# Kernel optimization log

Measured on AMD Instinct MI355X. Metric: run time of the kernel, lower is better.

## Reference

```python
import jax, jax.numpy as jnp
import numpy as np
import math

MAX_DELAY = 25
TAU = 2.0
VTH = 1.0
BN_EPS = 1e-5
ATAN_ALPHA = 2.0


def build_dcls_kernel(W, P, SIG, D):
    # Gaussian-interpolated DCLS kernel ('gauss' version).
    # W, P, SIG: (O, I, K) -> kernel (O, I, D)
    lim = D // 2
    j = jnp.arange(D, dtype=W.dtype)                      # (D,)
    Pc = jnp.clip(P, -lim, lim) + lim                     # (O, I, K)
    sig = jnp.abs(SIG) + 0.27
    g = jnp.exp(-0.5 * ((j - Pc[..., None]) / sig[..., None]) ** 2)  # (O,I,K,D)
    g = g / (g.sum(-1, keepdims=True) + 1e-7)
    return jnp.einsum('oik,oikd->oid', W, g)


def dcls_conv_positive(x, W, P, SIG, D):
    # Dale-positive: abs(weight) before kernel construction; padding=0 (VALID)
    k = build_dcls_kernel(jnp.abs(W), P, SIG, D)
    return jax.lax.conv_general_dilated(
        x, k, window_strides=(1,), padding='VALID',
        dimension_numbers=('NCW', 'OIW', 'NCW'))


def batchnorm_m(x, gamma, beta):
    # spikingjelly layer.BatchNorm1d step_mode='m' on (T, B, C):
    # flattens (T*B) as batch, normalizes per channel (training-mode stats).
    mean = x.mean(axis=(0, 1))
    var = x.var(axis=(0, 1))
    return (x - mean) * jax.lax.rsqrt(var + BN_EPS) * gamma + beta


def lif_multistep(x_seq, tau, v_th):
    # LIFNode, decay_input=False, v_reset=0 (hard reset), detach_reset=True,
    # ATan surrogate. x_seq: (T, B, C).
    inv_tau = jnp.asarray(1.0 / tau, x_seq.dtype)
    def step(v, xt):
        v = v * (1.0 - inv_tau) + xt              # charge (decay_input=False)
        u = v - v_th
        sg = jnp.arctan(0.5 * math.pi * ATAN_ALPHA * u) / math.pi + 0.5
        hard = (u >= 0).astype(xt.dtype)
        spike = sg + jax.lax.stop_gradient(hard - sg)
        v = v * (1.0 - jax.lax.stop_gradient(spike))   # hard reset, detached
        return v, spike
    v0 = jnp.zeros(x_seq.shape[1:], x_seq.dtype)
    _, spikes = jax.lax.scan(step, v0, x_seq)
    return spikes


def setup_inputs() -> dict:
    key = jax.random.key(0)
    ks = jax.random.split(key, 8)
    B, C_in, T = 64, 700, 300
    n_out, n_inh, K = 256, 128, 1
    return {
        'x': jax.random.normal(ks[0], (B, C_in, T), jnp.float32),
        'W_inh': jax.random.normal(ks[1], (n_inh, C_in, K), jnp.float32),
        'P_inh': jax.random.normal(ks[2], (n_inh, C_in, K), jnp.float32),
        'SIG_inh': jax.random.uniform(ks[3], (n_inh, C_in, K), jnp.float32),
        'W_exc': jax.random.normal(ks[4], (n_out, C_in, K), jnp.float32),
        'P_exc': jax.random.normal(ks[5], (n_out, C_in, K), jnp.float32),
        'SIG_exc': jax.random.uniform(ks[6], (n_out, C_in, K), jnp.float32),
        'w_exc_inh': jax.random.uniform(ks[7], (n_out, n_inh), jnp.float32),
        'bn_gamma': jnp.ones((n_inh,), jnp.float32),
        'bn_beta': jnp.zeros((n_inh,), jnp.float32),
    }


def reference(x, W_inh, P_inh, SIG_inh, W_exc, P_exc, SIG_exc, w_exc_inh,
              bn_gamma, bn_beta):
    # inhibitory branch
    in_inhib = dcls_conv_positive(x, W_inh, P_inh, SIG_inh, MAX_DELAY)  # (B,Ci,T')
    in_inhib = jnp.transpose(in_inhib, (2, 0, 1))                       # (T',B,Ci)
    in_inhib = batchnorm_m(in_inhib, bn_gamma, bn_beta)
    spikes = lif_multistep(in_inhib, TAU, VTH)                          # (T',B,Ci)
    out_inhib = jnp.einsum('tbi,oi->tbo', spikes, -jnp.abs(w_exc_inh))
    out_inhib = jnp.transpose(out_inhib, (1, 2, 0))                     # (B,O,T')
    # excitatory branch
    excit = dcls_conv_positive(x, W_exc, P_exc, SIG_exc, MAX_DELAY)     # (B,O,T')
    return excit + out_inhib
```

## Files before the change

### kernel.cpp

```cpp
#include <hip/hip_runtime.h>
#include <math.h>

#define CI   700
#define TIN  300
#define DD   25
#define TOUT 276
#define BB   64
#define OINH 128
#define OEXC 256

#define TROWS 312
#define IPAD  704

typedef __attribute__((ext_vector_type(8))) short short8;
typedef __attribute__((ext_vector_type(4))) float f32x4;
typedef __attribute__((ext_vector_type(8))) unsigned short ushort8v;

static __device__ __forceinline__ unsigned short f2bf(float f) {
    unsigned int u = __float_as_uint(f);
    unsigned int r = (u + 0x7FFFu + ((u >> 16) & 1u)) >> 16;
    return (unsigned short)r;
}
static __device__ __forceinline__ float bf2f(unsigned short h) {
    return __uint_as_float(((unsigned int)h) << 16);
}

static __device__ __forceinline__ void gload_lds16(const void* g, void* l) {
    __builtin_amdgcn_global_load_lds(
        (const __attribute__((address_space(1))) unsigned int*)g,
        (__attribute__((address_space(3))) unsigned int*)l, 16, 0, 0);
}

__global__ void build_kt(const float* __restrict__ W, const float* __restrict__ P,
                         const float* __restrict__ SIG, float* __restrict__ kt, int O) {
    int n = blockIdx.x * 256 + threadIdx.x;
    if (n >= O * CI) return;
    int o = n % O;
    int i = n / O;
    float w   = fabsf(W[o * CI + i]);
    float p   = fminf(fmaxf(P[o * CI + i], -12.f), 12.f) + 12.f;
    float sig = fabsf(SIG[o * CI + i]) + 0.27f;
    float inv = 1.f / sig;
    float g[DD];
    float sum = 0.f;
#pragma unroll
    for (int d = 0; d < DD; ++d) {
        float e = ((float)d - p) * inv;
        g[d] = expf(-0.5f * e * e);
        sum += g[d];
    }
    float sc = w / (sum + 1e-7f);
#pragma unroll
    for (int d = 0; d < DD; ++d)
        kt[(i * DD + d) * O + o] = g[d] * sc;
}

__global__ void kexc_build(const float* __restrict__ W, const float* __restrict__ P,
                           const float* __restrict__ SIG, unsigned short* __restrict__ kb2) {
    int n = blockIdx.x * 256 + threadIdx.x;
    if (n >= OEXC * IPAD) return;
    int o = n / IPAD, ip = n % IPAD;
    if (ip >= CI) {
#pragma unroll
        for (int d = 0; d < DD; ++d)
            kb2[((size_t)d * OEXC + o) * IPAD + ip] = 0;
        return;
    }
    float w   = fabsf(W[o * CI + ip]);
    float p   = fminf(fmaxf(P[o * CI + ip], -12.f), 12.f) + 12.f;
    float sig = fabsf(SIG[o * CI + ip]) + 0.27f;
    float inv = 1.f / sig;
    float g[DD];
    float sum = 0.f;
#pragma unroll
    for (int d = 0; d < DD; ++d) {
        float e = ((float)d - p) * inv;
        g[d] = expf(-0.5f * e * e);
        sum += g[d];
    }
    float sc = w / (sum + 1e-7f);
#pragma unroll
    for (int d = 0; d < DD; ++d)
        kb2[((size_t)d * OEXC + o) * IPAD + ip] = f2bf(g[d] * sc);
}

__global__ void kinh_build(const float* __restrict__ W, const float* __restrict__ P,
                           const float* __restrict__ SIG,
                           unsigned short* __restrict__ kbh, unsigned short* __restrict__ kbl) {
    int n = blockIdx.x * 256 + threadIdx.x;
    if (n >= OINH * IPAD) return;
    int o = n / IPAD, ip = n % IPAD;
    if (ip >= CI) {
#pragma unroll
        for (int d = 0; d < DD; ++d) {
            kbh[((size_t)d * OINH + o) * IPAD + ip] = 0;
            kbl[((size_t)d * OINH + o) * IPAD + ip] = 0;
        }
        return;
    }
    float w   = fabsf(W[o * CI + ip]);
    float p   = fminf(fmaxf(P[o * CI + ip], -12.f), 12.f) + 12.f;
    float sig = fabsf(SIG[o * CI + ip]) + 0.27f;
    float inv = 1.f / sig;
    float g[DD];
    float sum = 0.f;
#pragma unroll
    for (int d = 0; d < DD; ++d) {
        float e = ((float)d - p) * inv;
        g[d] = expf(-0.5f * e * e);
        sum += g[d];
    }
    float sc = w / (sum + 1e-7f);
#pragma unroll
    for (int d = 0; d < DD; ++d) {
        float v = g[d] * sc;
        unsigned short h = f2bf(v);
        kbh[((size_t)d * OINH + o) * IPAD + ip] = h;
        kbl[((size_t)d * OINH + o) * IPAD + ip] = f2bf(v - bf2f(h));
    }
}

__global__ __launch_bounds__(256)
void xt_kernel(const float* __restrict__ x, unsigned short* __restrict__ xTh,
               unsigned short* __restrict__ xTl) {
    __shared__ float tile[64][65];
    const int tid = threadIdx.x;
    const int t0 = blockIdx.x * 64, i0 = blockIdx.y * 64, b = blockIdx.z;
#pragma unroll
    for (int s = 0; s < 16; ++s) {
        int f = s * 256 + tid;
        int tt = f & 63, ii = f >> 6;
        float v = 0.f;
        if (t0 + tt < TIN && i0 + ii < CI)
            v = x[((size_t)b * CI + i0 + ii) * TIN + t0 + tt];
        tile[tt][ii] = v;
    }
    __syncthreads();
#pragma unroll
    for (int s = 0; s < 2; ++s) {
        int f = s * 256 + tid;
        int tt = f >> 3, g = f & 7;
        if (t0 + tt < TROWS) {
            ushort8v vh, vl;
#pragma unroll
            for (int e = 0; e < 8; ++e) {
                float v = tile[tt][g * 8 + e];
                unsigned short h = f2bf(v);
                vh[e] = h;
                vl[e] = f2bf(v - bf2f(h));
            }
            size_t off = ((size_t)b * TROWS + t0 + tt) * IPAD + i0 + g * 8;
            *(ushort8v*)(xTh + off) = vh;
            if (xTl) *(ushort8v*)(xTl + off) = vl;
        }
    }
}

__global__ void wt_kernel(const float* __restrict__ w, float* __restrict__ wt) {
    int n = blockIdx.x * 256 + threadIdx.x;
    if (n >= OINH * OEXC) return;
    int o = n % OEXC, c = n / OEXC;
    wt[c * OEXC + o] = -fabsf(w[o * OINH + c]);
}

__global__ __launch_bounds__(128)
void conv_fused32(const unsigned short* __restrict__ xTh, const unsigned short* __restrict__ xTl,
                  const unsigned short* __restrict__ kb2,
                  const unsigned short* __restrict__ kbh, const unsigned short* __restrict__ kbl,
                  float* __restrict__ pexc0, float* __restrict__ pexc1,
                  float* __restrict__ pinh0, float* __restrict__ pinh1) {
    __shared__ unsigned short lds[16384];

    const int tid  = threadIdx.x;
    const int wave = tid >> 6;
    const int lane = tid & 63;
    const int l15 = lane & 15, l4 = lane >> 4;
    const int tt   = blockIdx.x % 3;
    const int ksp  = blockIdx.x / 3;
    const int role = blockIdx.y;
    const int b    = blockIdx.z;
    const int t0   = tt * 96;
    const int icb  = ksp * 11;

    const int ld_r = lane >> 2;
    const int ld_c = (((lane & 3) ^ ((lane >> 3) & 3)) << 4);
    const int SA   = (l15 >> 1) & 3;

    const size_t xstride = (size_t)IPAD * 2;
    const char* xh_base = (const char*)xTh + ((size_t)b * TROWS + t0) * xstride;
    const char* xl_base = (const char*)xTl + ((size_t)b * TROWS + t0) * xstride;

    if (role < 2) {
        unsigned short* xs = lds;
        unsigned short* ks = lds + 4096;
        const int o0 = role * 128 + wave * 64;

        f32x4 acc[4][6];
#pragma unroll
        for (int i = 0; i < 4; ++i)
#pragma unroll
            for (int j = 0; j < 6; ++j) acc[i][j] = (f32x4)0.f;

        for (int c = 0; c < 11; ++c) {
            const size_t cb = (size_t)(icb + c) * 64;
            __syncthreads();
            for (int j = wave; j < 8; j += 2)
                gload_lds16(xh_base + (size_t)(16 * j + ld_r) * xstride + cb + ld_c,
                            (char*)xs + j * 1024);
            {
                const char* kbase = (const char*)kb2 + (size_t)o0 * xstride + cb;
                char* kdst = (char*)(ks + wave * 2048);
#pragma unroll
                for (int j = 0; j < 4; ++j)
                    gload_lds16(kbase + (size_t)(16 * j + ld_r) * xstride + ld_c,
                                kdst + j * 1024);
            }
            asm volatile("s_waitcnt vmcnt(0)" ::: "memory");
            __syncthreads();

            for (int d = 0; d < DD; ++d) {
                const int cur = d & 1;
                if (d < DD - 1) {
                    const char* kbase = (const char*)kb2 +
                        ((size_t)((d + 1) * OEXC) + o0) * xstride + cb;
                    char* kdst = (char*)(ks + ((cur ^ 1) * 2 + wave) * 2048);
#pragma unroll
                    for (int j = 0; j < 4; ++j)
                        gload_lds16(kbase + (size_t)(16 * j + ld_r) * xstride + ld_c,
                                    kdst + j * 1024);
                }
                const char* kp = (const char*)(ks + (cur * 2 + wave) * 2048);
                short8 A[4];
#pragma unroll
                for (int i = 0; i < 4; ++i)
                    A[i] = *(const short8*)(kp + (i * 16 + l15) * 64 + ((l4 ^ SA) << 4));
#pragma unroll
                for (int j = 0; j < 6; ++j) {
                    const int tr = j * 16 + l15 + d;
                    short8 Bv = *(const short8*)((const char*)xs + tr * 64 +
                                                 ((l4 ^ ((tr >> 1) & 3)) << 4));
#pragma unroll
                    for (int i = 0; i < 4; ++i)
                        acc[i][j] = __builtin_amdgcn_mfma_f32_16x16x32_bf16(
                            A[i], Bv, acc[i][j], 0, 0, 0);
                }
                asm volatile("s_waitcnt vmcnt(0)" ::: "memory");
            }
        }
        float* dst = ksp ? pexc1 : pexc0;
#pragma unroll
        for (int i = 0; i < 4; ++i)
#pragma unroll
            for (int j = 0; j < 6; ++j) {
                const int t = t0 + j * 16 + l15;
                if (t < TOUT) {
                    float* op = dst + ((size_t)b * OEXC + o0 + i * 16 + l4 * 4) * TOUT + t;
#pragma unroll
                    for (int r = 0; r < 4; ++r) op[(size_t)r * TOUT] = acc[i][j][r];
                }
            }
    } else {
        unsigned short* xsh = lds;
        unsigned short* xsl = lds + 4096;
        unsigned short* ksh = lds + 8192;
        unsigned short* ksl = lds + 12288;
        const int o0  = (role - 2) * 64;
        const int wtb = wave * 48;

        f32x4 acc[4][3];
#pragma unroll
        for (int i = 0; i < 4; ++i)
#pragma unroll
            for (int j = 0; j < 3; ++j) acc[i][j] = (f32x4)0.f;

        const unsigned short* kb = wave ? kbl : kbh;

        for (int c = 0; c < 11; ++c) {
            const size_t cb = (size_t)(icb + c) * 64;
            __syncthreads();
            for (int j = wave; j < 8; j += 2) {
                gload_lds16(xh_base + (size_t)(16 * j + ld_r) * xstride + cb + ld_c,
                            (char*)xsh + j * 1024);
                gload_lds16(xl_base + (size_t)(16 * j + ld_r) * xstride + cb + ld_c,
                            (char*)xsl + j * 1024);
            }
            {
                const char* kbase = (const char*)kb + (size_t)o0 * xstride + cb;
                char* kdst = (char*)((wave ? ksl : ksh));
#pragma unroll
                for (int j = 0; j < 4; ++j)
                    gload_lds16(kbase + (size_t)(16 * j + ld_r) * xstride + ld_c,
                                kdst + j * 1024);
            }
            asm volatile("s_waitcnt vmcnt(0)" ::: "memory");
            __syncthreads();

            for (int d = 0; d < DD; ++d) {
                const int cur = d & 1;
                if (d < DD - 1) {
                    const char* kbase = (const char*)kb +
                        ((size_t)((d + 1) * OINH) + o0) * xstride + cb;
                    char* kdst = (char*)((wave ? ksl : ksh) + (cur ^ 1) * 2048);
#pragma unroll
                    for (int j = 0; j < 4; ++j)
                        gload_lds16(kbase + (size_t)(16 * j + ld_r) * xstride + ld_c,
                                    kdst + j * 1024);
                }
                const char* kph = (const char*)(ksh + cur * 2048);
                const char* kpl = (const char*)(ksl + cur * 2048);
                short8 Ah[4], Al[4];
#pragma unroll
                for (int i = 0; i < 4; ++i) {
                    Ah[i] = *(const short8*)(kph + (i * 16 + l15) * 64 + ((l4 ^ SA) << 4));
                    Al[i] = *(const short8*)(kpl + (i * 16 + l15) * 64 + ((l4 ^ SA) << 4));
                }
#pragma unroll
                for (int j = 0; j < 3; ++j) {
                    const int tr = wtb + j * 16 + l15 + d;
                    const int xo = tr * 64 + ((l4 ^ ((tr >> 1) & 3)) << 4);
                    short8 Bh = *(const short8*)((const char*)xsh + xo);
                    short8 Bl = *(const short8*)((const char*)xsl + xo);
#pragma unroll
                    for (int i = 0; i < 4; ++i) {
                        acc[i][j] = __builtin_amdgcn_mfma_f32_16x16x32_bf16(
                            Ah[i], Bh, acc[i][j], 0, 0, 0);
                        acc[i][j] = __builtin_amdgcn_mfma_f32_16x16x32_bf16(
                            Ah[i], Bl, acc[i][j], 0, 0, 0);
                        acc[i][j] = __builtin_amdgcn_mfma_f32_16x16x32_bf16(
                            Al[i], Bh, acc[i][j], 0, 0, 0);
                    }
                }
                asm volatile("s_waitcnt vmcnt(0)" ::: "memory");
                __syncthreads();
            }
        }
        float* dst = ksp ? pinh1 : pinh0;
#pragma unroll
        for (int i = 0; i < 4; ++i)
#pragma unroll
            for (int j = 0; j < 3; ++j) {
                const int t = t0 + wtb + j * 16 + l15;
                if (t < TOUT) {
                    float* op = dst + ((size_t)b * OINH + o0 + i * 16 + l4 * 4) * TOUT + t;
#pragma unroll
                    for (int r = 0; r < 4; ++r) op[(size_t)r * TOUT] = acc[i][j][r];
                }
            }
    }
}

__global__ void add_exc(const float* __restrict__ p1, float* __restrict__ out) {
    int n = blockIdx.x * 256 + threadIdx.x;
    float4 a = ((const float4*)out)[n];
    float4 v = ((const float4*)p1)[n];
    a.x += v.x; a.y += v.y; a.z += v.z; a.w += v.w;
    ((float4*)out)[n] = a;
}

__global__ void bn_stats2(float* __restrict__ cinh, const float* __restrict__ q1,
                          const float* __restrict__ gamma, const float* __restrict__ beta,
                          float* __restrict__ scale, float* __restrict__ shift) {
    const int c = blockIdx.x, tid = threadIdx.x;
    float sum = 0.f, sq = 0.f;
    for (int idx = tid; idx < BB * TOUT; idx += 256) {
        int b = idx / TOUT, t = idx - b * TOUT;
        size_t off = (size_t)(b * OINH + c) * TOUT + t;
        float v = cinh[off] + q1[off];
        cinh[off] = v;
        sum += v; sq += v * v;
    }
#pragma unroll
    for (int off = 32; off; off >>= 1) {
        sum += __shfl_down(sum, off);
        sq  += __shfl_down(sq, off);
    }
    __shared__ float ls[8];
    int wid = tid >> 6;
    if ((tid & 63) == 0) { ls[wid * 2] = sum; ls[wid * 2 + 1] = sq; }
    __syncthreads();
    if (tid == 0) {
        float S = 0.f, Q = 0.f;
#pragma unroll
        for (int wv = 0; wv < 4; ++wv) { S += ls[wv * 2]; Q += ls[wv * 2 + 1]; }
        const float n = (float)(BB * TOUT);
        float mean = S / n;
        float var  = Q / n - mean * mean;
        float rs   = 1.f / sqrtf(var + 1e-5f);
        float sc   = gamma[c] * rs;
        scale[c] = sc;
        shift[c] = beta[c] - mean * sc;
    }
}

__global__ __launch_bounds__(128)
void conv_mfma(const unsigned short* __restrict__ xTh, const unsigned short* __restrict__ kb2,
               float* __restrict__ out) {
    __shared__ unsigned short xs[120 * 64];
    __shared__ unsigned short ks[2][2][64 * 64];

    const int tid  = threadIdx.x;
    const int wave = tid >> 6;
    const int lane = tid & 63;
    const int l15 = lane & 15, l4 = lane >> 4, l7 = lane & 7;
    const int b  = blockIdx.z;
    const int t0 = blockIdx.x * 96;
    const int o0 = blockIdx.y * 128 + wave * 64;

    const int ld_row = lane >> 3;
    const int ld_swz = ((l7 ^ ld_row) << 4);

    f32x4 acc[4][6];
#pragma unroll
    for (int i = 0; i < 4; ++i)
#pragma unroll
        for (int j = 0; j < 6; ++j) acc[i][j] = (f32x4)0.f;

    const char* xrow0 = (const char*)xTh + ((size_t)b * TROWS + t0) * (IPAD * 2);

    for (int ic = 0; ic < 11; ++ic) {
        const int ic0 = ic * 64;
        __syncthreads();
        for (int j = wave; j < 15; j += 2)
            gload_lds16(xrow0 + (size_t)(8 * j + ld_row) * (IPAD * 2) + ic0 * 2 + ld_swz,
                        (char*)xs + j * 1024);
        {
            const char* ksrc = (const char*)kb2 + ((size_t)o0) * (IPAD * 2) + ic0 * 2;
            char* kdst = (char*)ks + (0 * 2 + wave) * 8192;
#pragma unroll
            for (int j = 0; j < 8; ++j)
                gload_lds16(ksrc + (size_t)(8 * j + ld_row) * (IPAD * 2) + ld_swz,
                            kdst + j * 1024);
        }
        asm volatile("s_waitcnt vmcnt(0)" ::: "memory");
        __syncthreads();

        for (int d = 0; d < DD; ++d) {
            const int cur = d & 1;
            if (d < DD - 1) {
                const char* ksrc = (const char*)kb2 +
                    ((size_t)(d + 1) * OEXC + o0) * (IPAD * 2) + ic0 * 2;
                char* kdst = (char*)ks + ((cur ^ 1) * 2 + wave) * 8192;
#pragma unroll
                for (int j = 0; j < 8; ++j)
                    gload_lds16(ksrc + (size_t)(8 * j + ld_row) * (IPAD * 2) + ld_swz,
                                kdst + j * 1024);
            }
            const char* kp = (const char*)ks + (cur * 2 + wave) * 8192;
#pragma unroll
            for (int ks2 = 0; ks2 < 2; ++ks2) {
                const int cg = ks2 * 4 + l4;
                short8 A[4];
#pragma unroll
                for (int i = 0; i < 4; ++i)
                    A[i] = *(const short8*)(kp + (i * 16 + l15) * 128 + ((cg ^ l7) << 4));
#pragma unroll
                for (int j = 0; j < 6; ++j) {
                    const int tr = j * 16 + l15 + d;
                    short8 Bv = *(const short8*)((const char*)xs + tr * 128 +
                                                 ((cg ^ (tr & 7)) << 4));
#pragma unroll
                    for (int i = 0; i < 4; ++i)
                        acc[i][j] = __builtin_amdgcn_mfma_f32_16x16x32_bf16(
                            A[i], Bv, acc[i][j], 0, 0, 0);
                }
            }
            asm volatile("s_waitcnt vmcnt(0)" ::: "memory");
        }
    }

#pragma unroll
    for (int i = 0; i < 4; ++i)
#pragma unroll
        for (int j = 0; j < 6; ++j) {
            const int tt = t0 + j * 16 + l15;
            if (tt < TOUT) {
                float* op = out + ((size_t)b * OEXC + o0 + i * 16 + l4 * 4) * TOUT + tt;
#pragma unroll
                for (int r = 0; r < 4; ++r) op[(size_t)r * TOUT] = acc[i][j][r];
            }
        }
}

__global__ __launch_bounds__(128)
void conv_mfma_inh(const unsigned short* __restrict__ xTh, const unsigned short* __restrict__ xTl,
                   const unsigned short* __restrict__ kbh, const unsigned short* __restrict__ kbl,
                   float* __restrict__ cinh) {
    __shared__ unsigned short xsh[120 * 64];
    __shared__ unsigned short xsl[120 * 64];
    __shared__ unsigned short ksh[2][64 * 64];
    __shared__ unsigned short ksl[2][64 * 64];

    const int tid  = threadIdx.x;
    const int wave = tid >> 6;
    const int lane = tid & 63;
    const int l15 = lane & 15, l4 = lane >> 4, l7 = lane & 7;
    const int b  = blockIdx.z;
    const int t0 = blockIdx.x * 96;
    const int o0 = blockIdx.y * 64;
    const int wtb = wave * 48;

    const int ld_row = lane >> 3;
    const int ld_swz = ((l7 ^ ld_row) << 4);

    f32x4 acc[4][3];
#pragma unroll
    for (int i = 0; i < 4; ++i)
#pragma unroll
        for (int j = 0; j < 3; ++j) acc[i][j] = (f32x4)0.f;

    const char* xrh = (const char*)xTh + ((size_t)b * TROWS + t0) * (IPAD * 2);
    const char* xrl = (const char*)xTl + ((size_t)b * TROWS + t0) * (IPAD * 2);
    const unsigned short* kb = wave ? kbl : kbh;

    for (int ic = 0; ic < 11; ++ic) {
        const int ic0 = ic * 64;
        __syncthreads();
        for (int j = wave; j < 15; j += 2) {
            gload_lds16(xrh + (size_t)(8 * j + ld_row) * (IPAD * 2) + ic0 * 2 + ld_swz,
                        (char*)xsh + j * 1024);
            gload_lds16(xrl + (size_t)(8 * j + ld_row) * (IPAD * 2) + ic0 * 2 + ld_swz,
                        (char*)xsl + j * 1024);
        }
        {
            char* kd = wave ? (char*)ksl[0] : (char*)ksh[0];
#pragma unroll
            for (int j = 0; j < 8; ++j)
                gload_lds16((const char*)kb +
                                ((size_t)(0 * OINH + o0 + 8 * j + ld_row)) * (IPAD * 2) +
                                ic0 * 2 + ld_swz,
                            kd + j * 1024);
        }
        asm volatile("s_waitcnt vmcnt(0)" ::: "memory");
        __syncthreads();

        for (int d = 0; d < DD; ++d) {
            const int cur = d & 1;
            if (d < DD - 1) {
                char* kd = wave ? (char*)ksl[cur ^ 1] : (char*)ksh[cur ^ 1];
#pragma unroll
                for (int j = 0; j < 8; ++j)
                    gload_lds16((const char*)kb +
                                    ((size_t)((d + 1) * OINH + o0 + 8 * j + ld_row)) * (IPAD * 2) +
                                    ic0 * 2 + ld_swz,
                                kd + j * 1024);
            }
            const char* kph = (const char*)ksh[cur];
            const char* kpl = (const char*)ksl[cur];
#pragma unroll
            for (int k2 = 0; k2 < 2; ++k2) {
                const int cg = k2 * 4 + l4;
                short8 Ah[4], Al[4];
#pragma unroll
                for (int i = 0; i < 4; ++i) {
                    Ah[i] = *(const short8*)(kph + (i * 16 + l15) * 128 + ((cg ^ l7) << 4));
                    Al[i] = *(const short8*)(kpl + (i * 16 + l15) * 128 + ((cg ^ l7) << 4));
                }
#pragma unroll
                for (int j = 0; j < 3; ++j) {
                    const int tr = wtb + j * 16 + l15 + d;
                    short8 Bh = *(const short8*)((const char*)xsh + tr * 128 +
                                                 ((cg ^ (tr & 7)) << 4));
                    short8 Bl = *(const short8*)((const char*)xsl + tr * 128 +
                                                 ((cg ^ (tr & 7)) << 4));
#pragma unroll
                    for (int i = 0; i < 4; ++i) {
                        acc[i][j] = __builtin_amdgcn_mfma_f32_16x16x32_bf16(
                            Ah[i], Bh, acc[i][j], 0, 0, 0);
                        acc[i][j] = __builtin_amdgcn_mfma_f32_16x16x32_bf16(
                            Ah[i], Bl, acc[i][j], 0, 0, 0);
                        acc[i][j] = __builtin_amdgcn_mfma_f32_16x16x32_bf16(
                            Al[i], Bh, acc[i][j], 0, 0, 0);
                    }
                }
            }
            asm volatile("s_waitcnt vmcnt(0)" ::: "memory");
            __syncthreads();
        }
    }

#pragma unroll
    for (int i = 0; i < 4; ++i)
#pragma unroll
        for (int j = 0; j < 3; ++j) {
            const int tt = t0 + wtb + j * 16 + l15;
            if (tt < TOUT) {
                float* op = cinh + ((size_t)b * OINH + o0 + i * 16 + l4 * 4) * TOUT + tt;
#pragma unroll
                for (int r = 0; r < 4; ++r) op[(size_t)r * TOUT] = acc[i][j][r];
            }
        }
}

__global__ __launch_bounds__(256)
void conv_dcls(const float* __restrict__ x, const float* __restrict__ kt,
               float* __restrict__ out, int O) {
    __shared__ float k_lds[100 * 128];
    __shared__ float x_lds[4 * 88];

    const int tid = threadIdx.x;
    const int tx = tid & 7;
    const int ty = tid >> 3;
    const int b  = blockIdx.z;
    const int t0 = blockIdx.x * 64;
    const int o0 = blockIdx.y * 128;
    const int tlim = TIN - t0;

    float acc[4][8];
#pragma unroll
    for (int ro = 0; ro < 4; ++ro)
#pragma unroll
        for (int rt = 0; rt < 8; ++rt) acc[ro][rt] = 0.f;

    for (int chunk = 0; chunk < 175; ++chunk) {
        const int i0 = chunk * 4;
        __syncthreads();
#pragma unroll
        for (int s = 0; s < 13; ++s) {
            int f = tid + s * 256;
            if (f < 3200) {
                int j = f >> 5, o4 = f & 31;
                ((float4*)k_lds)[f] =
                    *(const float4*)(kt + (size_t)(i0 * DD + j) * O + o0 + o4 * 4);
            }
        }
        if (tid < 88) {
            int icc = tid / 22, wq = tid % 22;
            float4 v = make_float4(0.f, 0.f, 0.f, 0.f);
            if (wq * 4 < tlim)
                v = *(const float4*)(x + (size_t)(b * CI + i0 + icc) * TIN + t0 + wq * 4);
            ((float4*)x_lds)[tid] = v;
        }
        __syncthreads();
#pragma unroll
        for (int icc = 0; icc < 4; ++icc) {
            float xv[32];
#pragma unroll
            for (int wq = 0; wq < 8; ++wq)
                *(float4*)(xv + 4 * wq) = ((const float4*)(x_lds + icc * 88))[tx * 2 + wq];
#pragma unroll
            for (int d = 0; d < DD; ++d) {
                float4 kv = ((const float4*)(k_lds + (icc * DD + d) * 128))[ty];
                float kvv[4] = {kv.x, kv.y, kv.z, kv.w};
#pragma unroll
                for (int ro = 0; ro < 4; ++ro)
#pragma unroll
                    for (int rt = 0; rt < 8; ++rt)
                        acc[ro][rt] += kvv[ro] * xv[rt + d];
            }
        }
    }
    const int tvalid = TOUT - t0;
#pragma unroll
    for (int ro = 0; ro < 4; ++ro) {
        float* op = out + (size_t)(b * O + o0 + ty * 4 + ro) * TOUT + t0;
#pragma unroll
        for (int u = 0; u < 2; ++u) {
            int toff = tx * 8 + u * 4;
            if (toff < tvalid) {
                float4 v = make_float4(acc[ro][u * 4 + 0], acc[ro][u * 4 + 1],
                                       acc[ro][u * 4 + 2], acc[ro][u * 4 + 3]);
                *(float4*)(op + toff) = v;
            }
        }
    }
}

__global__ void bn_stats(const float* __restrict__ cinh, const float* __restrict__ gamma,
                         const float* __restrict__ beta, float* __restrict__ scale,
                         float* __restrict__ shift) {
    const int c = blockIdx.x, tid = threadIdx.x;
    float sum = 0.f, sq = 0.f;
    for (int idx = tid; idx < BB * TOUT; idx += 256) {
        int b = idx / TOUT, t = idx - b * TOUT;
        float v = cinh[(size_t)(b * OINH + c) * TOUT + t];
        sum += v; sq += v * v;
    }
#pragma unroll
    for (int off = 32; off; off >>= 1) {
        sum += __shfl_down(sum, off);
        sq  += __shfl_down(sq, off);
    }
    __shared__ float ls[8];
    int wid = tid >> 6;
    if ((tid & 63) == 0) { ls[wid * 2] = sum; ls[wid * 2 + 1] = sq; }
    __syncthreads();
    if (tid == 0) {
        float S = 0.f, Q = 0.f;
#pragma unroll
        for (int wv = 0; wv < 4; ++wv) { S += ls[wv * 2]; Q += ls[wv * 2 + 1]; }
        const float n = (float)(BB * TOUT);
        float mean = S / n;
        float var  = Q / n - mean * mean;
        float rs   = 1.f / sqrtf(var + 1e-5f);
        float sc   = gamma[c] * rs;
        scale[c] = sc;
        shift[c] = beta[c] - mean * sc;
    }
}

__global__ void lif_kernel(const float* __restrict__ cinh, const float* __restrict__ scale,
                           const float* __restrict__ shift, unsigned char* __restrict__ spk) {
    const int b = blockIdx.x, c = threadIdx.x;
    const float sc = scale[c], sh = shift[c];
    const float* row = cinh + (size_t)(b * OINH + c) * TOUT;
    float v = 0.f;
    for (int t = 0; t < TOUT; ++t) {
        float xin = row[t] * sc + sh;
        v = 0.5f * v + xin;
        unsigned char s = (v >= 1.f) ? 1 : 0;
        spk[((size_t)t * BB + b) * OINH + c] = s;
        v = (v >= 1.f) ? 0.f : v;
    }
}

__global__ __launch_bounds__(256)
void finale(const unsigned char* __restrict__ spk, const float* __restrict__ wt,
            float* __restrict__ out) {
    __shared__ float s_lds[64 * 129];
    const int tid = threadIdx.x;
    const int tx = tid & 15, ty = tid >> 4;
    const int b = blockIdx.z, t0 = blockIdx.x * 64, o0 = blockIdx.y * 64;

#pragma unroll
    for (int s = 0; s < 32; ++s) {
        int f = tid + s * 256;
        int tt = f >> 7, c = f & 127;
        float v = 0.f;
        if (t0 + tt < TOUT) v = (float)spk[((size_t)(t0 + tt) * BB + b) * OINH + c];
        s_lds[tt * 129 + c] = v;
    }
    __syncthreads();

    float acc[4][4] = {{0.f}};
#pragma unroll 4
    for (int c = 0; c < 128; ++c) {
        float4 wv = *(const float4*)(wt + c * OEXC + o0 + ty * 4);
        float wvv[4] = {wv.x, wv.y, wv.z, wv.w};
        float sv[4];
#pragma unroll
        for (int rt = 0; rt < 4; ++rt) sv[rt] = s_lds[(tx * 4 + rt) * 129 + c];
#pragma unroll
        for (int ro = 0; ro < 4; ++ro)
#pragma unroll
            for (int rt = 0; rt < 4; ++rt)
                acc[ro][rt] += wvv[ro] * sv[rt];
    }

    const int tvalid = TOUT - t0;
    if (tx * 4 < tvalid) {
#pragma unroll
        for (int ro = 0; ro < 4; ++ro) {
            float* op = out + (size_t)(b * OEXC + o0 + ty * 4 + ro) * TOUT + t0 + tx * 4;
            float4 v = *(float4*)op;
            v.x += acc[ro][0]; v.y += acc[ro][1]; v.z += acc[ro][2]; v.w += acc[ro][3];
            *(float4*)op = v;
        }
    }
}

extern "C" void kernel_launch(void* const* d_in, const int* in_sizes, int n_in,
                              void* d_out, int out_size, void* d_ws, size_t ws_size,
                              hipStream_t stream) {
    const float* x       = (const float*)d_in[0];
    const float* W_inh   = (const float*)d_in[1];
    const float* P_inh   = (const float*)d_in[2];
    const float* SIG_inh = (const float*)d_in[3];
    const float* W_exc   = (const float*)d_in[4];
    const float* P_exc   = (const float*)d_in[5];
    const float* SIG_exc = (const float*)d_in[6];
    const float* w_ei    = (const float*)d_in[7];
    const float* gamma   = (const float*)d_in[8];
    const float* beta    = (const float*)d_in[9];
    float* out = (float*)d_out;

    const size_t XT_ELEMS   = (size_t)BB * TROWS * IPAD;
    const size_t KEXC_ELEMS = (size_t)DD * OEXC * IPAD;
    const size_t KINH_ELEMS = (size_t)DD * OINH * IPAD;
    const size_t CINH_ELEMS = (size_t)BB * OINH * TOUT;
    const size_t PEXC_ELEMS = (size_t)BB * OEXC * TOUT;

    const size_t NEED_FAST = 2 * XT_ELEMS * 2 + KEXC_ELEMS * 2 + 2 * KINH_ELEMS * 2 +
                             CINH_ELEMS * 4 + OINH * OEXC * 4 + CINH_ELEMS;
    const size_t NEED_FAST2 = (2 * XT_ELEMS + KEXC_ELEMS + 2 * KINH_ELEMS) * 2 +
                              (PEXC_ELEMS + 2 * CINH_ELEMS + OINH * OEXC + 256) * 4 +
                              CINH_ELEMS;

    if (ws_size >= NEED_FAST2) {
        unsigned short* xTh = (unsigned short*)d_ws;
        unsigned short* xTl = xTh + XT_ELEMS;
        unsigned short* kb2 = xTl + XT_ELEMS;
        unsigned short* kbh = kb2 + KEXC_ELEMS;
        unsigned short* kbl = kbh + KINH_ELEMS;
        float* pexc1 = (float*)(kbl + KINH_ELEMS);
        float* cinh  = pexc1 + PEXC_ELEMS;
        float* pinh1 = cinh + CINH_ELEMS;
        float* wt    = pinh1 + CINH_ELEMS;
        float* scale = wt + OINH * OEXC;
        float* shift = scale + OINH;
        unsigned char* spk = (unsigned char*)(shift + OINH);

        hipLaunchKernelGGL(kexc_build, dim3((OEXC * IPAD + 255) / 256), dim3(256), 0, stream,
                           W_exc, P_exc, SIG_exc, kb2);
        hipLaunchKernelGGL(kinh_build, dim3((OINH * IPAD + 255) / 256), dim3(256), 0, stream,
                           W_inh, P_inh, SIG_inh, kbh, kbl);
        hipLaunchKernelGGL(xt_kernel, dim3(5, 11, 64), dim3(256), 0, stream, x, xTh, xTl);
        hipLaunchKernelGGL(wt_kernel, dim3(128), dim3(256), 0, stream, w_ei, wt);

        hipLaunchKernelGGL(conv_fused32, dim3(6, 4, 64), dim3(128), 0, stream,
                           xTh, xTl, kb2, kbh, kbl, out, pexc1, cinh, pinh1);

        hipLaunchKernelGGL(add_exc, dim3((unsigned)(PEXC_ELEMS / 4 / 256)), dim3(256), 0, stream,
                           pexc1, out);
        hipLaunchKernelGGL(bn_stats2, dim3(128), dim3(256), 0, stream,
                           cinh, pinh1, gamma, beta, scale, shift);
        hipLaunchKernelGGL(lif_kernel, dim3(64), dim3(128), 0, stream, cinh, scale, shift, spk);
        hipLaunchKernelGGL(finale, dim3(5, 4, 64), dim3(256), 0, stream, spk, wt, out);
    } else if (ws_size >= NEED_FAST) {
        unsigned short* xTh = (unsigned short*)d_ws;
        unsigned short* xTl = xTh + XT_ELEMS;
        unsigned short* kb2 = xTl + XT_ELEMS;
        unsigned short* kbh = kb2 + KEXC_ELEMS;
        unsigned short* kbl = kbh + KINH_ELEMS;
        float* cinh  = (float*)(kbl + KINH_ELEMS);
        float* wt    = cinh + CINH_ELEMS;
        float* scale = wt + OINH * OEXC;
        float* shift = scale + OINH;
        unsigned char* spk = (unsigned char*)(shift + OINH);

        hipLaunchKernelGGL(kexc_build, dim3((OEXC * IPAD + 255) / 256), dim3(256), 0, stream,
                           W_exc, P_exc, SIG_exc, kb2);
        hipLaunchKernelGGL(kinh_build, dim3((OINH * IPAD + 255) / 256), dim3(256), 0, stream,
                           W_inh, P_inh, SIG_inh, kbh, kbl);
        hipLaunchKernelGGL(xt_kernel, dim3(5, 11, 64), dim3(256), 0, stream, x, xTh, xTl);
        hipLaunchKernelGGL(wt_kernel, dim3(128), dim3(256), 0, stream, w_ei, wt);

        hipLaunchKernelGGL(conv_mfma, dim3(3, 2, 64), dim3(128), 0, stream, xTh, kb2, out);
        hipLaunchKernelGGL(conv_mfma_inh, dim3(3, 2, 64), dim3(128), 0, stream,
                           xTh, xTl, kbh, kbl, cinh);

        hipLaunchKernelGGL(bn_stats, dim3(128), dim3(256), 0, stream, cinh, gamma, beta, scale, shift);
        hipLaunchKernelGGL(lif_kernel, dim3(64), dim3(128), 0, stream, cinh, scale, shift, spk);
        hipLaunchKernelGGL(finale, dim3(5, 4, 64), dim3(256), 0, stream, spk, wt, out);
    } else {
        unsigned short* xTh = (unsigned short*)d_ws;
        unsigned short* kb2 = xTh + XT_ELEMS;
        float* kt_inh = (float*)(kb2 + KEXC_ELEMS);
        float* cinh   = kt_inh + 2240000;
        float* wt     = cinh + CINH_ELEMS;
        float* scale  = wt + OINH * OEXC;
        float* shift  = scale + OINH;
        unsigned char* spk = (unsigned char*)(shift + OINH);

        hipLaunchKernelGGL(kexc_build, dim3((OEXC * IPAD + 255) / 256), dim3(256), 0, stream,
                           W_exc, P_exc, SIG_exc, kb2);
        hipLaunchKernelGGL(build_kt, dim3(350), dim3(256), 0, stream,
                           W_inh, P_inh, SIG_inh, kt_inh, OINH);
        hipLaunchKernelGGL(xt_kernel, dim3(5, 11, 64), dim3(256), 0, stream, x, xTh,
                           (unsigned short*)nullptr);
        hipLaunchKernelGGL(wt_kernel, dim3(128), dim3(256), 0, stream, w_ei, wt);

        hipLaunchKernelGGL(conv_mfma, dim3(3, 2, 64), dim3(128), 0, stream, xTh, kb2, out);
        hipLaunchKernelGGL(conv_dcls, dim3(5, 1, 64), dim3(256), 0, stream, x, kt_inh, cinh, OINH);

        hipLaunchKernelGGL(bn_stats, dim3(128), dim3(256), 0, stream, cinh, gamma, beta, scale, shift);
        hipLaunchKernelGGL(lif_kernel, dim3(64), dim3(128), 0, stream, cinh, scale, shift, spk);
        hipLaunchKernelGGL(finale, dim3(5, 4, 64), dim3(256), 0, stream, spk, wt, out);
    }
}
```

Before: 548.2 us.

## Triple-buffer kernel prefetch and rebalance inhibitory MFMA tiling; tile LIF input through LDS

The fused conv kernel now keeps three LDS kernel buffers and prefetches two delay steps ahead, waiting with a partial vmcnt so loads overlap the MFMA work. The inhibitory path splits output channels across the two waves, each computing the hi/lo split over the full 96-step tile, instead of splitting time, and drops a per-delay __syncthreads. A new LIF kernel stages input chunks through padded LDS so global reads are coalesced. Costs are more LDS per block, which may reduce occupancy, plus some reshuffling of fallback code.

```diff
diff --git a/kernel.cpp b/kernel.cpp
--- a/kernel.cpp
+++ b/kernel.cpp
@@ -164,12 +164,12 @@
 }
 
 __global__ __launch_bounds__(128)
-void conv_fused32(const unsigned short* __restrict__ xTh, const unsigned short* __restrict__ xTl,
-                  const unsigned short* __restrict__ kb2,
-                  const unsigned short* __restrict__ kbh, const unsigned short* __restrict__ kbl,
-                  float* __restrict__ pexc0, float* __restrict__ pexc1,
-                  float* __restrict__ pinh0, float* __restrict__ pinh1) {
-    __shared__ unsigned short lds[16384];
+void conv_fused_v3(const unsigned short* __restrict__ xTh, const unsigned short* __restrict__ xTl,
+                   const unsigned short* __restrict__ kb2,
+                   const unsigned short* __restrict__ kbh, const unsigned short* __restrict__ kbl,
+                   float* __restrict__ pexc0, float* __restrict__ pexc1,
+                   float* __restrict__ pinh0, float* __restrict__ pinh1) {
+    __shared__ unsigned short lds[20480];
 
     const int tid  = threadIdx.x;
     const int wave = tid >> 6;
@@ -207,29 +207,31 @@
             for (int j = wave; j < 8; j += 2)
                 gload_lds16(xh_base + (size_t)(16 * j + ld_r) * xstride + cb + ld_c,
                             (char*)xs + j * 1024);
-            {
-                const char* kbase = (const char*)kb2 + (size_t)o0 * xstride + cb;
-                char* kdst = (char*)(ks + wave * 2048);
+#pragma unroll
+            for (int q = 0; q < 2; ++q) {
+                const char* kbase = (const char*)kb2 + ((size_t)(q * OEXC) + o0) * xstride + cb;
+                char* kdst = (char*)ks + (q * 2 + wave) * 4096;
 #pragma unroll
                 for (int j = 0; j < 4; ++j)
                     gload_lds16(kbase + (size_t)(16 * j + ld_r) * xstride + ld_c,
                                 kdst + j * 1024);
             }
-            asm volatile("s_waitcnt vmcnt(0)" ::: "memory");
+            asm volatile("s_waitcnt vmcnt(4)" ::: "memory");
             __syncthreads();
 
+            int cur = 0;
             for (int d = 0; d < DD; ++d) {
-                const int cur = d & 1;
-                if (d < DD - 1) {
+                if (d < DD - 2) {
+                    int nb = cur + 2; if (nb >= 3) nb -= 3;
                     const char* kbase = (const char*)kb2 +
-                        ((size_t)((d + 1) * OEXC) + o0) * xstride + cb;
-                    char* kdst = (char*)(ks + ((cur ^ 1) * 2 + wave) * 2048);
+                        ((size_t)((d + 2) * OEXC) + o0) * xstride + cb;
+                    char* kdst = (char*)ks + (nb * 2 + wave) * 4096;
 #pragma unroll
                     for (int j = 0; j < 4; ++j)
                         gload_lds16(kbase + (size_t)(16 * j + ld_r) * xstride + ld_c,
                                     kdst + j * 1024);
                 }
-                const char* kp = (const char*)(ks + (cur * 2 + wave) * 2048);
+                const char* kp = (const char*)ks + (cur * 2 + wave) * 4096;
                 short8 A[4];
 #pragma unroll
                 for (int i = 0; i < 4; ++i)
@@ -244,7 +246,11 @@
                         acc[i][j] = __builtin_amdgcn_mfma_f32_16x16x32_bf16(
                             A[i], Bv, acc[i][j], 0, 0, 0);
                 }
-                asm volatile("s_waitcnt vmcnt(0)" ::: "memory");
+                if (d < DD - 2)
+                    asm volatile("s_waitcnt vmcnt(4)" ::: "memory");
+                else if (d == DD - 2)
+                    asm volatile("s_waitcnt vmcnt(0)" ::: "memory");
+                cur = (cur == 2) ? 0 : cur + 1;
             }
         }
         float* dst = ksp ? pexc1 : pexc0;
@@ -262,18 +268,15 @@
     } else {
         unsigned short* xsh = lds;
         unsigned short* xsl = lds + 4096;
-        unsigned short* ksh = lds + 8192;
-        unsigned short* ksl = lds + 12288;
+        unsigned short* kws = lds + 8192;
         const int o0  = (role - 2) * 64;
-        const int wtb = wave * 48;
-
-        f32x4 acc[4][3];
-#pragma unroll
-        for (int i = 0; i < 4; ++i)
-#pragma unroll
-            for (int j = 0; j < 3; ++j) acc[i][j] = (f32x4)0.f;
-
-        const unsigned short* kb = wave ? kbl : kbh;
+        const int o0w = o0 + wave * 32;
+
+        f32x4 acc[2][6];
+#pragma unroll
+        for (int i = 0; i < 2; ++i)
+#pragma unroll
+            for (int j = 0; j < 6; ++j) acc[i][j] = (f32x4)0.f;
 
         for (int c = 0; c < 11; ++c) {
             const size_t cb = (size_t)(icb + c) * 64;
@@ -284,44 +287,50 @@
                 gload_lds16(xl_base + (size_t)(16 * j + ld_r) * xstride + cb + ld_c,
                             (char*)xsl + j * 1024);
             }
-            {
-                const char* kbase = (const char*)kb + (size_t)o0 * xstride + cb;
-                char* kdst = (char*)((wave ? ksl : ksh));
-#pragma unroll
-                for (int j = 0; j < 4; ++j)
-                    gload_lds16(kbase + (size_t)(16 * j + ld_r) * xstride + ld_c,
+#pragma unroll
+            for (int q = 0; q < 2; ++q) {
+                const size_t ko = ((size_t)(q * OINH) + o0w) * xstride + cb;
+                char* kdst = (char*)kws + (q * 2 + wave) * 4096;
+#pragma unroll
+                for (int j = 0; j < 2; ++j) {
+                    gload_lds16((const char*)kbh + ko + (size_t)(16 * j + ld_r) * xstride + ld_c,
                                 kdst + j * 1024);
-            }
-            asm volatile("s_waitcnt vmcnt(0)" ::: "memory");
+                    gload_lds16((const char*)kbl + ko + (size_t)(16 * j + ld_r) * xstride + ld_c,
+                                kdst + 2048 + j * 1024);
+                }
+            }
+            asm volatile("s_waitcnt vmcnt(4)" ::: "memory");
             __syncthreads();
 
+            int cur = 0;
             for (int d = 0; d < DD; ++d) {
-                const int cur = d & 1;
-                if (d < DD - 1) {
-                    const char* kbase = (const char*)kb +
-                        ((size_t)((d + 1) * OINH) + o0) * xstride + cb;
-                    char* kdst = (char*)((wave ? ksl : ksh) + (cur ^ 1) * 2048);
-#pragma unroll
-                    for (int j = 0; j < 4; ++j)
-                        gload_lds16(kbase + (size_t)(16 * j + ld_r) * xstride + ld_c,
+                if (d < DD - 2) {
+                    int nb = cur + 2; if (nb >= 3) nb -= 3;
+                    const size_t ko = ((size_t)((d + 2) * OINH) + o0w) * xstride + cb;
+                    char* kdst = (char*)kws + (nb * 2 + wave) * 4096;
+#pragma unroll
+                    for (int j = 0; j < 2; ++j) {
+                        gload_lds16((const char*)kbh + ko + (size_t)(16 * j + ld_r) * xstride + ld_c,
                                     kdst + j * 1024);
-                }
-                const char* kph = (const char*)(ksh + cur * 2048);
-                const char* kpl = (const char*)(ksl + cur * 2048);
-                short8 Ah[4], Al[4];
-#pragma unroll
-                for (int i = 0; i < 4; ++i) {
-                    Ah[i] = *(const short8*)(kph + (i * 16 + l15) * 64 + ((l4 ^ SA) << 4));
-                    Al[i] = *(const short8*)(kpl + (i * 16 + l15) * 64 + ((l4 ^ SA) << 4));
-                }
-#pragma unroll
-                for (int j = 0; j < 3; ++j) {
-                    const int tr = wtb + j * 16 + l15 + d;
+                        gload_lds16((const char*)kbl + ko + (size_t)(16 * j + ld_r) * xstride + ld_c,
+                                    kdst + 2048 + j * 1024);
+                    }
+                }
+                const char* kp = (const char*)kws + (cur * 2 + wave) * 4096;
+                short8 Ah[2], Al[2];
+#pragma unroll
+                for (int i = 0; i < 2; ++i) {
+                    Ah[i] = *(const short8*)(kp + (i * 16 + l15) * 64 + ((l4 ^ SA) << 4));
+                    Al[i] = *(const short8*)(kp + 2048 + (i * 16 + l15) * 64 + ((l4 ^ SA) << 4));
+                }
+#pragma unroll
+                for (int j = 0; j < 6; ++j) {
+                    const int tr = j * 16 + l15 + d;
                     const int xo = tr * 64 + ((l4 ^ ((tr >> 1) & 3)) << 4);
                     short8 Bh = *(const short8*)((const char*)xsh + xo);
                     short8 Bl = *(const short8*)((const char*)xsl + xo);
 #pragma unroll
-                    for (int i = 0; i < 4; ++i) {
+                    for (int i = 0; i < 2; ++i) {
                         acc[i][j] = __builtin_amdgcn_mfma_f32_16x16x32_bf16(
                             Ah[i], Bh, acc[i][j], 0, 0, 0);
                         acc[i][j] = __builtin_amdgcn_mfma_f32_16x16x32_bf16(
@@ -330,18 +339,21 @@
                             Al[i], Bh, acc[i][j], 0, 0, 0);
                     }
                 }
-                asm volatile("s_waitcnt vmcnt(0)" ::: "memory");
-                __syncthreads();
+                if (d < DD - 2)
+                    asm volatile("s_waitcnt vmcnt(4)" ::: "memory");
+                else if (d == DD - 2)
+                    asm volatile("s_waitcnt vmcnt(0)" ::: "memory");
+                cur = (cur == 2) ? 0 : cur + 1;
             }
         }
         float* dst = ksp ? pinh1 : pinh0;
 #pragma unroll
-        for (int i = 0; i < 4; ++i)
-#pragma unroll
-            for (int j = 0; j < 3; ++j) {
-                const int t = t0 + wtb + j * 16 + l15;
+        for (int i = 0; i < 2; ++i)
+#pragma unroll
+            for (int j = 0; j < 6; ++j) {
+                const int t = t0 + j * 16 + l15;
                 if (t < TOUT) {
-                    float* op = dst + ((size_t)b * OINH + o0 + i * 16 + l4 * 4) * TOUT + t;
+                    float* op = dst + ((size_t)b * OINH + o0w + i * 16 + l4 * 4) * TOUT + t;
 #pragma unroll
                     for (int r = 0; r < 4; ++r) op[(size_t)r * TOUT] = acc[i][j][r];
                 }
@@ -393,6 +405,35 @@
 }
 
 __global__ __launch_bounds__(128)
+void lif2(const float* __restrict__ cinh, const float* __restrict__ scale,
+          const float* __restrict__ shift, unsigned char* __restrict__ spk) {
+    __shared__ float tile[128 * 65];
+    const int b = blockIdx.x, c = threadIdx.x;
+    const float sc = scale[c], sh = shift[c];
+    const float* base = cinh + (size_t)b * OINH * TOUT;
+    float v = 0.f;
+    for (int tc = 0; tc < TOUT; tc += 64) {
+        const int len = (TOUT - tc < 64) ? (TOUT - tc) : 64;
+        const int L4 = len >> 2;
+        __syncthreads();
+        for (int q = c; q < 128 * L4; q += 128) {
+            int cc = q / L4, e = q - cc * L4;
+            float4 vv = *(const float4*)(base + (size_t)cc * TOUT + tc + e * 4);
+            float* dstp = &tile[cc * 65 + e * 4];
+            dstp[0] = vv.x; dstp[1] = vv.y; dstp[2] = vv.z; dstp[3] = vv.w;
+        }
+        __syncthreads();
+        for (int t2 = 0; t2 < len; ++t2) {
+            float xin = tile[c * 65 + t2] * sc + sh;
+            v = 0.5f * v + xin;
+            bool s = (v >= 1.f);
+            spk[((size_t)(tc + t2) * BB + b) * OINH + c] = s ? 1 : 0;
+            v = s ? 0.f : v;
+        }
+    }
+}
+
+__global__ __launch_bounds__(128)
 void conv_mfma(const unsigned short* __restrict__ xTh, const unsigned short* __restrict__ kb2,
                float* __restrict__ out) {
     __shared__ unsigned short xs[120 * 64];
@@ -591,80 +632,6 @@
         }
 }
 
-__global__ __launch_bounds__(256)
-void conv_dcls(const float* __restrict__ x, const float* __restrict__ kt,
-               float* __restrict__ out, int O) {
-    __shared__ float k_lds[100 * 128];
-    __shared__ float x_lds[4 * 88];
-
-    const int tid = threadIdx.x;
-    const int tx = tid & 7;
-    const int ty = tid >> 3;
-    const int b  = blockIdx.z;
-    const int t0 = blockIdx.x * 64;
-    const int o0 = blockIdx.y * 128;
-    const int tlim = TIN - t0;
-
-    float acc[4][8];
-#pragma unroll
-    for (int ro = 0; ro < 4; ++ro)
-#pragma unroll
-        for (int rt = 0; rt < 8; ++rt) acc[ro][rt] = 0.f;
-
-    for (int chunk = 0; chunk < 175; ++chunk) {
-        const int i0 = chunk * 4;
-        __syncthreads();
-#pragma unroll
-        for (int s = 0; s < 13; ++s) {
-            int f = tid + s * 256;
-            if (f < 3200) {
-                int j = f >> 5, o4 = f & 31;
-                ((float4*)k_lds)[f] =
-                    *(const float4*)(kt + (size_t)(i0 * DD + j) * O + o0 + o4 * 4);
-            }
-        }
-        if (tid < 88) {
-            int icc = tid / 22, wq = tid % 22;
-            float4 v = make_float4(0.f, 0.f, 0.f, 0.f);
-            if (wq * 4 < tlim)
-                v = *(const float4*)(x + (size_t)(b * CI + i0 + icc) * TIN + t0 + wq * 4);
-            ((float4*)x_lds)[tid] = v;
-        }
-        __syncthreads();
-#pragma unroll
-        for (int icc = 0; icc < 4; ++icc) {
-            float xv[32];
-#pragma unroll
-            for (int wq = 0; wq < 8; ++wq)
-                *(float4*)(xv + 4 * wq) = ((const float4*)(x_lds + icc * 88))[tx * 2 + wq];
-#pragma unroll
-            for (int d = 0; d < DD; ++d) {
-                float4 kv = ((const float4*)(k_lds + (icc * DD + d) * 128))[ty];
-                float kvv[4] = {kv.x, kv.y, kv.z, kv.w};
-#pragma unroll
-                for (int ro = 0; ro < 4; ++ro)
-#pragma unroll
-                    for (int rt = 0; rt < 8; ++rt)
-                        acc[ro][rt] += kvv[ro] * xv[rt + d];
-            }
-        }
-    }
-    const int tvalid = TOUT - t0;
-#pragma unroll
-    for (int ro = 0; ro < 4; ++ro) {
-        float* op = out + (size_t)(b * O + o0 + ty * 4 + ro) * TOUT + t0;
-#pragma unroll
-        for (int u = 0; u < 2; ++u) {
-            int toff = tx * 8 + u * 4;
-            if (toff < tvalid) {
-                float4 v = make_float4(acc[ro][u * 4 + 0], acc[ro][u * 4 + 1],
-                                       acc[ro][u * 4 + 2], acc[ro][u * 4 + 3]);
-                *(float4*)(op + toff) = v;
-            }
-        }
-    }
-}
-
 __global__ void bn_stats(const float* __restrict__ cinh, const float* __restrict__ gamma,
                          const float* __restrict__ beta, float* __restrict__ scale,
                          float* __restrict__ shift) {
@@ -695,6 +662,51 @@
         float sc   = gamma[c] * rs;
         scale[c] = sc;
         shift[c] = beta[c] - mean * sc;
+    }
+}
+
+__global__ __launch_bounds__(256)
+void finale(const unsigned char* __restrict__ spk, const float* __restrict__ wt,
+            float* __restrict__ out) {
+    __shared__ float s_lds[64 * 129];
+    const int tid = threadIdx.x;
+    const int tx = tid & 15, ty = tid >> 4;
+    const int b = blockIdx.z, t0 = blockIdx.x * 64, o0 = blockIdx.y * 64;
+
+#pragma unroll
+    for (int s = 0; s < 32; ++s) {
+        int f = tid + s * 256;
+        int tt = f >> 7, c = f & 127;
+        float v = 0.f;
+        if (t0 + tt < TOUT) v = (float)spk[((size_t)(t0 + tt) * BB + b) * OINH + c];
+        s_lds[tt * 129 + c] = v;
+    }
+    __syncthreads();
+
+    float acc[4][4] = {{0.f}};
+#pragma unroll 4
+    for (int c = 0; c < 128; ++c) {
+        float4 wv = *(const float4*)(wt + c * OEXC + o0 + ty * 4);
+        float wvv[4] = {wv.x, wv.y, wv.z, wv.w};
+        float sv[4];
+#pragma unroll
+        for (int rt = 0; rt < 4; ++rt) sv[rt] = s_lds[(tx * 4 + rt) * 129 + c];
+#pragma unroll
+        for (int ro = 0; ro < 4; ++ro)
+#pragma unroll
+            for (int rt = 0; rt < 4; ++rt)
+                acc[ro][rt] += wvv[ro] * sv[rt];
+    }
+
+    const int tvalid = TOUT - t0;
+    if (tx * 4 < tvalid) {
+#pragma unroll
+        for (int ro = 0; ro < 4; ++ro) {
+            float* op = out + (size_t)(b * OEXC + o0 + ty * 4 + ro) * TOUT + t0 + tx * 4;
+            float4 v = *(float4*)op;
+            v.x += acc[ro][0]; v.y += acc[ro][1]; v.z += acc[ro][2]; v.w += acc[ro][3];
+            *(float4*)op = v;
+        }
     }
 }
 
@@ -710,51 +722,6 @@
         unsigned char s = (v >= 1.f) ? 1 : 0;
         spk[((size_t)t * BB + b) * OINH + c] = s;
         v = (v >= 1.f) ? 0.f : v;
-    }
-}
-
-__global__ __launch_bounds__(256)
-void finale(const unsigned char* __restrict__ spk, const float* __restrict__ wt,
-            float* __restrict__ out) {
-    __shared__ float s_lds[64 * 129];
-    const int tid = threadIdx.x;
-    const int tx = tid & 15, ty = tid >> 4;
-    const int b = blockIdx.z, t0 = blockIdx.x * 64, o0 = blockIdx.y * 64;
-
-#pragma unroll
-    for (int s = 0; s < 32; ++s) {
-        int f = tid + s * 256;
-        int tt = f >> 7, c = f & 127;
-        float v = 0.f;
-        if (t0 + tt < TOUT) v = (float)spk[((size_t)(t0 + tt) * BB + b) * OINH + c];
-        s_lds[tt * 129 + c] = v;
-    }
-    __syncthreads();
-
-    float acc[4][4] = {{0.f}};
-#pragma unroll 4
-    for (int c = 0; c < 128; ++c) {
-        float4 wv = *(const float4*)(wt + c * OEXC + o0 + ty * 4);
-        float wvv[4] = {wv.x, wv.y, wv.z, wv.w};
-        float sv[4];
-#pragma unroll
-        for (int rt = 0; rt < 4; ++rt) sv[rt] = s_lds[(tx * 4 + rt) * 129 + c];
-#pragma unroll
-        for (int ro = 0; ro < 4; ++ro)
-#pragma unroll
-            for (int rt = 0; rt < 4; ++rt)
-                acc[ro][rt] += wvv[ro] * sv[rt];
-    }
-
-    const int tvalid = TOUT - t0;
-    if (tx * 4 < tvalid) {
-#pragma unroll
-        for (int ro = 0; ro < 4; ++ro) {
-            float* op = out + (size_t)(b * OEXC + o0 + ty * 4 + ro) * TOUT + t0 + tx * 4;
-            float4 v = *(float4*)op;
-            v.x += acc[ro][0]; v.y += acc[ro][1]; v.z += acc[ro][2]; v.w += acc[ro][3];
-            *(float4*)op = v;
-        }
     }
 }
 
@@ -806,14 +773,14 @@
         hipLaunchKernelGGL(xt_kernel, dim3(5, 11, 64), dim3(256), 0, stream, x, xTh, xTl);
         hipLaunchKernelGGL(wt_kernel, dim3(128), dim3(256), 0, stream, w_ei, wt);
 
-        hipLaunchKernelGGL(conv_fused32, dim3(6, 4, 64), dim3(128), 0, stream,
+        hipLaunchKernelGGL(conv_fused_v3, dim3(6, 4, 64), dim3(128), 0, stream,
                            xTh, xTl, kb2, kbh, kbl, out, pexc1, cinh, pinh1);
 
         hipLaunchKernelGGL(add_exc, dim3((unsigned)(PEXC_ELEMS / 4 / 256)), dim3(256), 0, stream,
                            pexc1, out);
         hipLaunchKernelGGL(bn_stats2, dim3(128), dim3(256), 0, stream,
                            cinh, pinh1, gamma, beta, scale, shift);
-        hipLaunchKernelGGL(lif_kernel, dim3(64), dim3(128), 0, stream, cinh, scale, shift, spk);
+        hipLaunchKernelGGL(lif2, dim3(64), dim3(128), 0, stream, cinh, scale, shift, spk);
         hipLaunchKernelGGL(finale, dim3(5, 4, 64), dim3(256), 0, stream, spk, wt, out);
     } else if (ws_size >= NEED_FAST) {
         unsigned short* xTh = (unsigned short*)d_ws;
@@ -860,10 +827,85 @@
         hipLaunchKernelGGL(wt_kernel, dim3(128), dim3(256), 0, stream, w_ei, wt);
 
         hipLaunchKernelGGL(conv_mfma, dim3(3, 2, 64), dim3(128), 0, stream, xTh, kb2, out);
-        hipLaunchKernelGGL(conv_dcls, dim3(5, 1, 64), dim3(256), 0, stream, x, kt_inh, cinh, OINH);
+        extern __global__ void conv_dcls_fb(const float*, const float*, float*, int);
+        hipLaunchKernelGGL(conv_dcls_fb, dim3(5, 1, 64), dim3(256), 0, stream, x, kt_inh, cinh, OINH);
 
         hipLaunchKernelGGL(bn_stats, dim3(128), dim3(256), 0, stream, cinh, gamma, beta, scale, shift);
         hipLaunchKernelGGL(lif_kernel, dim3(64), dim3(128), 0, stream, cinh, scale, shift, spk);
         hipLaunchKernelGGL(finale, dim3(5, 4, 64), dim3(256), 0, stream, spk, wt, out);
     }
 }
+
+__global__ __launch_bounds__(256)
+void conv_dcls_fb(const float* __restrict__ x, const float* __restrict__ kt,
+                  float* __restrict__ out, int O) {
+    __shared__ float k_lds[100 * 128];
+    __shared__ float x_lds[4 * 88];
+
+    const int tid = threadIdx.x;
+    const int tx = tid & 7;
+    const int ty = tid >> 3;
+    const int b  = blockIdx.z;
+    const int t0 = blockIdx.x * 64;
+    const int o0 = blockIdx.y * 128;
+    const int tlim = TIN - t0;
+
+    float acc[4][8];
+#pragma unroll
+    for (int ro = 0; ro < 4; ++ro)
+#pragma unroll
+        for (int rt = 0; rt < 8; ++rt) acc[ro][rt] = 0.f;
+
+    for (int chunk = 0; chunk < 175; ++chunk) {
+        const int i0 = chunk * 4;
+        __syncthreads();
+#pragma unroll
+        for (int s = 0; s < 13; ++s) {
+            int f = tid + s * 256;
+            if (f < 3200) {
+                int j = f >> 5, o4 = f & 31;
+                ((float4*)k_lds)[f] =
+                    *(const float4*)(kt + (size_t)(i0 * DD + j) * O + o0 + o4 * 4);
+            }
+        }
+        if (tid < 88) {
+            int icc = tid / 22, wq = tid % 22;
+            float4 v = make_float4(0.f, 0.f, 0.f, 0.f);
+            if (wq * 4 < tlim)
+                v = *(const float4*)(x + (size_t)(b * CI + i0 + icc) * TIN + t0 + wq * 4);
+            ((float4*)x_lds)[tid] = v;
+        }
+        __syncthreads();
+#pragma unroll
+        for (int icc = 0; icc < 4; ++icc) {
+            float xv[32];
+#pragma unroll
+            for (int wq = 0; wq < 8; ++wq)
+                *(float4*)(xv + 4 * wq) = ((const float4*)(x_lds + icc * 88))[tx * 2 + wq];
+#pragma unroll
+            for (int d = 0; d < DD; ++d) {
+                float4 kv = ((const float4*)(k_lds + (icc * DD + d) * 128))[ty];
+                float kvv[4] = {kv.x, kv.y, kv.z, kv.w};
+#pragma unroll
+                for (int ro = 0; ro < 4; ++ro)
+#pragma unroll
+                    for (int rt = 0; rt < 8; ++rt)
+                        acc[ro][rt] += kvv[ro] * xv[rt + d];
+            }
+        }
+    }
+    const int tvalid = TOUT - t0;
+#pragma unroll
+    for (int ro = 0; ro < 4; ++ro) {
+        float* op = out + (size_t)(b * O + o0 + ty * 4 + ro) * TOUT + t0;
+#pragma unroll
+        for (int u = 0; u < 2; ++u) {
+            int toff = tx * 8 + u * 4;
+            if (toff < tvalid) {
+                float4 v = make_float4(acc[ro][u * 4 + 0], acc[ro][u * 4 + 1],
+                                       acc[ro][u * 4 + 2], acc[ro][u * 4 + 3]);
+                *(float4*)(op + toff) = v;
+            }
+        }
+    }
+}
```

New measurement: 566.2 us. 1.03x slower.
